# Optimization experiments

Measured on AMD Instinct MI355X. Metric: run time of the kernel, lower is better.

Reference implementation:

```python
import jax, jax.numpy as jnp
import numpy as np

D = 196; NCH = 64; H = 8; DH = 64; INNER = H * DH; MLP = 784; SEQ = 65


def _ln(x, g, b, eps=1e-5):
    m = x.mean(-1, keepdims=True)
    v = x.var(-1, keepdims=True)
    return (x - m) / jnp.sqrt(v + eps) * g + b


def setup_inputs() -> dict:
    key = jax.random.key(0)
    ks = jax.random.split(key, 12)
    f = jax.random.normal
    return dict(
        x=f(ks[0], (1, SEQ, D), dtype=jnp.float32),
        tokens=f(ks[1], (1, D), dtype=jnp.float32),
        x_pe=f(ks[2], (1, NCH, D), dtype=jnp.float32),
        conv_k=f(ks[3], (3, 3), dtype=jnp.float32) * 0.3,   # Conv2d(1,1,3) kernel
        bn_g=jnp.ones(()), bn_b=jnp.zeros(()), bn_rm=jnp.zeros(()), bn_rv=jnp.ones(()),
        fc_w1=f(ks[4], (NCH, 12)) * 0.1,
        fc_w2=f(ks[5], (12, NCH)) * 0.1,
        ln1_g=jnp.ones((D,)), ln1_b=jnp.zeros((D,)),
        ln2_g=jnp.ones((D,)), ln2_b=jnp.zeros((D,)),
        w_qkv=f(ks[6], (D, 3 * INNER)) * 0.05,
        w_out=f(ks[7], (INNER, D)) * 0.05, b_out=jnp.zeros((D,)),
        ff_w1=f(ks[8], (D, MLP)) * 0.05, ff_b1=jnp.zeros((MLP,)),
        ff_w2=f(ks[9], (MLP, D)) * 0.05, ff_b2=jnp.zeros((D,)),
    )


def reference(x, tokens, x_pe, conv_k, bn_g, bn_b, bn_rm, bn_rv,
              fc_w1, fc_w2, ln1_g, ln1_b, ln2_g, ln2_b,
              w_qkv, w_out, b_out, ff_w1, ff_b1, ff_w2, ff_b2):
    # --- per-channel Conv2d(1,1,3,p=1)+BN+ReLU, batched over all 64 rows ---
    # Each row is (1,1,1,196): height 1 with pad 1 means the top/bottom kernel
    # rows only touch zero padding, so only the middle kernel row contributes
    # -> equivalent to a 1D conv with kernel conv_k[1].
    rows = x_pe[0]                      # [64,196]
    km = conv_k[1]                      # [3]
    xp = jnp.pad(rows, ((0, 0), (1, 1)))
    conv = km[0] * xp[:, :D] + km[1] * xp[:, 1:D + 1] + km[2] * xp[:, 2:D + 2]
    bn = (conv - bn_rm) / jnp.sqrt(bn_rv + 1e-5) * bn_g + bn_b
    a = jax.nn.relu(bn)                 # [64,196]  (== x_AfterConv / a)

    # --- sort-based suppress/excitation channel gating ---
    b1 = a.mean(-1)                     # [64] adaptive avg pool
    val = jnp.sort(b1)
    idx = jnp.argsort(b1)
    middle = jnp.where((val.max() < 0) | (val.min() > 0),
                       jnp.int32(32), jnp.argmax(val > 0).astype(jnp.int32))
    rank = jnp.argsort(idx)             # rank of each channel in ascending order
    sup = rank < middle                 # channels in idx[:middle]
    l_s = middle.astype(b1.dtype)
    l_e = (NCH - middle).astype(b1.dtype)
    b2 = jnp.where(sup,
                   b1 - 1.0 / (1.0 + jnp.power(l_s, b1)),
                   b1 + 1.0 / (1.0 + jnp.power(l_e, -b1)))

    c = jax.nn.sigmoid(jax.nn.relu(b2 @ fc_w1) @ fc_w2)   # [64]
    x_att = a * c[:, None]                                  # [64,196]
    x_att = jnp.concatenate([x_att, tokens.reshape(1, D)], axis=0)[None]  # [1,65,196]

    # --- PreNorm attention ---
    h = _ln(x, ln1_g, ln1_b)
    qkv = h @ w_qkv
    q, k, v = jnp.split(qkv, 3, axis=-1)
    def heads(t):
        return t.reshape(1, SEQ, H, DH).transpose(0, 2, 1, 3)  # b h n d
    q, k, v = heads(q), heads(k), heads(v)
    attn = jax.nn.softmax(jnp.einsum('bhnd,bhmd->bhnm', q, k) * (DH ** -0.5), axis=-1)
    o = jnp.einsum('bhnm,bhmd->bhnd', attn, v).transpose(0, 2, 1, 3).reshape(1, SEQ, INNER)
    x = o @ w_out + b_out + x + x_att

    # --- PreNorm feed-forward ---
    h2 = _ln(x, ln2_g, ln2_b)
    x = (jax.nn.gelu(h2 @ ff_w1 + ff_b1, approximate=False) @ ff_w2 + ff_b2) + x
    return x
```

## Files before the change

### kernel.cpp

```cpp
#include <hip/hip_runtime.h>
#include <math.h>

#define D 196
#define NCH 64
#define NH 8
#define DHD 64
#define INNER 512
#define MLP 784
#define SEQ 65

__device__ __forceinline__ float bsum(float v, float* red) {
    for (int off = 32; off > 0; off >>= 1) v += __shfl_down(v, off, 64);
    int lane = threadIdx.x & 63, wid = threadIdx.x >> 6;
    if (lane == 0) red[wid] = v;
    __syncthreads();
    float s = red[0] + red[1] + red[2] + red[3];
    __syncthreads();
    return s;
}

__global__ void __launch_bounds__(256) k1(const float* __restrict__ x_pe,
        const float* __restrict__ conv_k, const float* __restrict__ bn_g,
        const float* __restrict__ bn_b, const float* __restrict__ bn_rm,
        const float* __restrict__ bn_rv, const float* __restrict__ x,
        const float* __restrict__ ln1_g, const float* __restrict__ ln1_b,
        const float* __restrict__ w_qkv,
        float* __restrict__ a, float* __restrict__ b1, float* __restrict__ qkv,
        float* __restrict__ x2, float* __restrict__ out) {
    __shared__ float red[4];
    __shared__ float h[D];
    __shared__ float ps[256];
    int b = blockIdx.x, t = threadIdx.x;
    if (b < NCH) {
        const float* row = x_pe + b * D;
        float val = 0.f;
        if (t < D) {
            float km0 = conv_k[3], km1 = conv_k[4], km2 = conv_k[5];
            float inv = rsqrtf(bn_rv[0] + 1e-5f);
            float l = (t > 0) ? row[t - 1] : 0.f;
            float m = row[t];
            float r = (t < D - 1) ? row[t + 1] : 0.f;
            float conv = km0 * l + km1 * m + km2 * r;
            float bn = (conv - bn_rm[0]) * inv * bn_g[0] + bn_b[0];
            val = fmaxf(bn, 0.f);
            a[b * D + t] = val;
        }
        float tot = bsum(val, red);
        if (t == 0) b1[b] = tot * (1.f / (float)D);
    } else if (b < 844) {
        int qb = b - NCH;
        int n = qb / 12, cg = qb % 12;
        const float* row = x + n * D;
        float v = (t < D) ? row[t] : 0.f;
        float mean = bsum(v, red) * (1.f / (float)D);
        float d = (t < D) ? (v - mean) : 0.f;
        float var = bsum(d * d, red) * (1.f / (float)D);
        float rinv = rsqrtf(var + 1e-5f);
        if (t < D) h[t] = d * rinv * ln1_g[t] + ln1_b[t];
        __syncthreads();
        int half = t >> 7, lt = t & 127;
        int col = cg * 128 + lt;
        const float* wp = w_qkv + (half * 98) * 1536 + col;
        const float* hp = h + half * 98;
        float acc = 0.f;
#pragma unroll 14
        for (int i = 0; i < 98; i++) acc += hp[i] * wp[i * 1536];
        ps[t] = acc;
        __syncthreads();
        if (t < 128) qkv[n * 1536 + cg * 128 + t] = ps[t] + ps[t + 128];
    } else {
        for (int i = t; i < SEQ * D; i += 256) { x2[i] = 0.f; out[i] = 0.f; }
    }
}

__global__ void __launch_bounds__(256) k2(const float* __restrict__ b1,
        const float* __restrict__ fc_w1, const float* __restrict__ fc_w2,
        const float* __restrict__ qkv, float* __restrict__ c, float* __restrict__ o) {
    __shared__ float smem[544];
    int b = blockIdx.x, t = threadIdx.x;
    if (b == 0) {
        float* sb1 = smem;
        float* sb2 = smem + 64;
        float* hid = smem + 128;
        if (t < NCH) sb1[t] = b1[t];
        __syncthreads();
        if (t < NCH) {
            float v = sb1[t];
            float mx = -1e30f, mn = 1e30f;
            int cle = 0, rank = 0;
            for (int j = 0; j < NCH; j++) {
                float w = sb1[j];
                mx = fmaxf(mx, w);
                mn = fminf(mn, w);
                if (w <= 0.f) cle++;
                if (w < v || (w == v && j < t)) rank++;
            }
            int middle;
            if (mx < 0.f || mn > 0.f) middle = 32;
            else if (mx <= 0.f) middle = 0;
            else middle = cle;
            float b2;
            if (rank < middle) {
                float ls = (float)middle;
                b2 = v - 1.f / (1.f + powf(ls, v));
            } else {
                float le = (float)(NCH - middle);
                b2 = v + 1.f / (1.f + powf(le, -v));
            }
            sb2[t] = b2;
        }
        __syncthreads();
        if (t < 12) {
            float s = 0.f;
            for (int j = 0; j < NCH; j++) s += sb2[j] * fc_w1[j * 12 + t];
            hid[t] = fmaxf(s, 0.f);
        }
        __syncthreads();
        if (t < NCH) {
            float s = 0.f;
            for (int k = 0; k < 12; k++) s += hid[k] * fc_w2[k * NCH + t];
            c[t] = 1.f / (1.f + expf(-s));
        }
    } else {
        int w = t >> 6, lane = t & 63;
        int task = (b - 1) * 4 + w;
        int n = task >> 3, hh = task & 7;
        float* q = smem + w * 64;
        float* pp = smem + 256 + w * 66;
        q[lane] = qkv[n * 1536 + hh * DHD + lane];
        __syncthreads();
        const float4* q4 = (const float4*)q;
        const float scale = 0.125f;
        for (int m = lane; m < SEQ; m += 64) {
            const float4* kr = (const float4*)(qkv + m * 1536 + INNER + hh * DHD);
            float s = 0.f;
#pragma unroll
            for (int i = 0; i < 16; i++) {
                float4 kv = kr[i];
                float4 qv = q4[i];
                s += qv.x * kv.x + qv.y * kv.y + qv.z * kv.z + qv.w * kv.w;
            }
            pp[m] = s * scale;
        }
        __syncthreads();
        float mx = -1e30f;
#pragma unroll 5
        for (int m = 0; m < SEQ; m++) mx = fmaxf(mx, pp[m]);
        __syncthreads();
        for (int m = lane; m < SEQ; m += 64) pp[m] = expf(pp[m] - mx);
        __syncthreads();
        float sum = 0.f;
#pragma unroll 5
        for (int m = 0; m < SEQ; m++) sum += pp[m];
        float rs = 1.f / sum;
        float acc = 0.f;
#pragma unroll 8
        for (int m = 0; m < SEQ; m++)
            acc += pp[m] * qkv[m * 1536 + 2 * INNER + hh * DHD + lane];
        o[n * INNER + hh * DHD + lane] = acc * rs;
    }
}

__global__ void __launch_bounds__(256) k3(const float* __restrict__ o,
        const float* __restrict__ w_out, const float* __restrict__ b_out,
        const float* __restrict__ x, const float* __restrict__ a,
        const float* __restrict__ c, const float* __restrict__ tokens,
        float* __restrict__ x2) {
    __shared__ float st[128];
    int n = blockIdx.x, kc = blockIdx.y, t = threadIdx.x;
    if (t < 128) st[t] = o[n * INNER + kc * 128 + t];
    __syncthreads();
    if (t < D) {
        const float* wp = w_out + (kc * 128) * D + t;
        float acc = 0.f;
#pragma unroll 16
        for (int i = 0; i < 128; i++) acc += st[i] * wp[i * D];
        if (kc == 0) {
            float att = (n < NCH) ? a[n * D + t] * c[n] : tokens[t];
            acc += b_out[t] + x[n * D + t] + att;
        }
        atomicAdd(&x2[n * D + t], acc);
    }
}

__global__ void __launch_bounds__(256) k4(const float* __restrict__ x2,
        const float* __restrict__ ln2_g, const float* __restrict__ ln2_b,
        const float* __restrict__ ff_w1, const float* __restrict__ ff_b1,
        float* __restrict__ tb) {
    __shared__ float red[4];
    __shared__ float h[D];
    __shared__ float ps[256];
    int n = blockIdx.x, cg = blockIdx.y, t = threadIdx.x;
    const float* row = x2 + n * D;
    float v = (t < D) ? row[t] : 0.f;
    float mean = bsum(v, red) * (1.f / (float)D);
    float d = (t < D) ? (v - mean) : 0.f;
    float var = bsum(d * d, red) * (1.f / (float)D);
    float rinv = rsqrtf(var + 1e-5f);
    if (t < D) h[t] = d * rinv * ln2_g[t] + ln2_b[t];
    __syncthreads();
    int half = t >> 7, lt = t & 127;
    float acc = 0.f;
    if (lt < 98) {
        int col = cg * 98 + lt;
        const float* wp = ff_w1 + (half * 98) * MLP + col;
        const float* hp = h + half * 98;
        acc = (half == 0) ? ff_b1[col] : 0.f;
#pragma unroll 14
        for (int i = 0; i < 98; i++) acc += hp[i] * wp[i * MLP];
    }
    ps[t] = acc;
    __syncthreads();
    if (t < 98) {
        float s = ps[t] + ps[t + 128];
        float gl = 0.5f * s * (1.f + erff(s * 0.70710678118f));
        tb[n * MLP + cg * 98 + t] = gl;
    }
}

__global__ void __launch_bounds__(256) k5(const float* __restrict__ tb,
        const float* __restrict__ ff_w2, const float* __restrict__ ff_b2,
        const float* __restrict__ x2, float* __restrict__ out) {
    __shared__ float st[98];
    int n = blockIdx.x, kc = blockIdx.y, t = threadIdx.x;
    if (t < 98) st[t] = tb[n * MLP + kc * 98 + t];
    __syncthreads();
    if (t < D) {
        const float* wp = ff_w2 + (kc * 98) * D + t;
        float acc = 0.f;
#pragma unroll 14
        for (int i = 0; i < 98; i++) acc += st[i] * wp[i * D];
        if (kc == 0) acc += ff_b2[t] + x2[n * D + t];
        atomicAdd(&out[n * D + t], acc);
    }
}

extern "C" void kernel_launch(void* const* d_in, const int* in_sizes, int n_in,
                              void* d_out, int out_size, void* d_ws, size_t ws_size,
                              hipStream_t stream) {
    const float* x      = (const float*)d_in[0];
    const float* tokens = (const float*)d_in[1];
    const float* x_pe   = (const float*)d_in[2];
    const float* conv_k = (const float*)d_in[3];
    const float* bn_g   = (const float*)d_in[4];
    const float* bn_b   = (const float*)d_in[5];
    const float* bn_rm  = (const float*)d_in[6];
    const float* bn_rv  = (const float*)d_in[7];
    const float* fc_w1  = (const float*)d_in[8];
    const float* fc_w2  = (const float*)d_in[9];
    const float* ln1_g  = (const float*)d_in[10];
    const float* ln1_b  = (const float*)d_in[11];
    const float* ln2_g  = (const float*)d_in[12];
    const float* ln2_b  = (const float*)d_in[13];
    const float* w_qkv  = (const float*)d_in[14];
    const float* w_out  = (const float*)d_in[15];
    const float* b_out  = (const float*)d_in[16];
    const float* ff_w1  = (const float*)d_in[17];
    const float* ff_b1  = (const float*)d_in[18];
    const float* ff_w2  = (const float*)d_in[19];
    const float* ff_b2  = (const float*)d_in[20];
    float* out = (float*)d_out;

    float* ws = (float*)d_ws;
    float* a    = ws;
    float* b1   = ws + 12544;
    float* cc   = ws + 12608;
    float* qkv  = ws + 12672;
    float* o    = ws + 112512;
    float* x2   = ws + 145792;
    float* tb   = ws + 158532;

    k1<<<845, 256, 0, stream>>>(x_pe, conv_k, bn_g, bn_b, bn_rm, bn_rv,
                                x, ln1_g, ln1_b, w_qkv, a, b1, qkv, x2, out);
    k2<<<131, 256, 0, stream>>>(b1, fc_w1, fc_w2, qkv, cc, o);
    k3<<<dim3(SEQ, 4), 256, 0, stream>>>(o, w_out, b_out, x, a, cc, tokens, x2);
    k4<<<dim3(SEQ, 8), 256, 0, stream>>>(x2, ln2_g, ln2_b, ff_w1, ff_b1, tb);
    k5<<<dim3(SEQ, 8), 256, 0, stream>>>(tb, ff_w2, ff_b2, x2, out);
}
```

Before: 130.7 us.

## Fuse attention with output projection and vectorize GEMV loops with float2

```diff
diff --git a/kernel.cpp b/kernel.cpp
--- a/kernel.cpp
+++ b/kernel.cpp
@@ -26,12 +26,14 @@
         const float* __restrict__ ln1_g, const float* __restrict__ ln1_b,
         const float* __restrict__ w_qkv,
         float* __restrict__ a, float* __restrict__ b1, float* __restrict__ qkv,
-        float* __restrict__ x2, float* __restrict__ out) {
+        float* __restrict__ out) {
     __shared__ float red[4];
     __shared__ float h[D];
-    __shared__ float ps[256];
+    __shared__ float ps[512];
     int b = blockIdx.x, t = threadIdx.x;
     if (b < NCH) {
+        int zi = b * 200 + t;
+        if (t < 200 && zi < SEQ * D) out[zi] = 0.f;
         const float* row = x_pe + b * D;
         float val = 0.f;
         if (t < D) {
@@ -47,7 +49,7 @@
         }
         float tot = bsum(val, red);
         if (t == 0) b1[b] = tot * (1.f / (float)D);
-    } else if (b < 844) {
+    } else {
         int qb = b - NCH;
         int n = qb / 12, cg = qb % 12;
         const float* row = x + n * D;
@@ -58,30 +60,40 @@
         float rinv = rsqrtf(var + 1e-5f);
         if (t < D) h[t] = d * rinv * ln1_g[t] + ln1_b[t];
         __syncthreads();
-        int half = t >> 7, lt = t & 127;
-        int col = cg * 128 + lt;
-        const float* wp = w_qkv + (half * 98) * 1536 + col;
-        const float* hp = h + half * 98;
-        float acc = 0.f;
-#pragma unroll 14
-        for (int i = 0; i < 98; i++) acc += hp[i] * wp[i * 1536];
-        ps[t] = acc;
-        __syncthreads();
-        if (t < 128) qkv[n * 1536 + cg * 128 + t] = ps[t] + ps[t + 128];
-    } else {
-        for (int i = t; i < SEQ * D; i += 256) { x2[i] = 0.f; out[i] = 0.f; }
-    }
-}
-
-__global__ void __launch_bounds__(256) k2(const float* __restrict__ b1,
+        int qq = t >> 6, lt = t & 63;
+        int c0 = cg * 128 + lt * 2;
+        const float* wp = w_qkv + (qq * 49) * 1536 + c0;
+        const float* hp = h + qq * 49;
+        float a0 = 0.f, a1 = 0.f;
+#pragma unroll
+        for (int i = 0; i < 49; i++) {
+            float2 w2 = *(const float2*)(wp + i * 1536);
+            float hv = hp[i];
+            a0 += hv * w2.x;
+            a1 += hv * w2.y;
+        }
+        ps[qq * 128 + lt * 2] = a0;
+        ps[qq * 128 + lt * 2 + 1] = a1;
+        __syncthreads();
+        if (t < 64) {
+            float s0 = ps[t * 2] + ps[128 + t * 2] + ps[256 + t * 2] + ps[384 + t * 2];
+            float s1 = ps[t * 2 + 1] + ps[129 + t * 2] + ps[257 + t * 2] + ps[385 + t * 2];
+            float2 o2 = make_float2(s0, s1);
+            *(float2*)(qkv + n * 1536 + cg * 128 + t * 2) = o2;
+        }
+    }
+}
+
+__global__ void __launch_bounds__(512) k2(const float* __restrict__ b1,
         const float* __restrict__ fc_w1, const float* __restrict__ fc_w2,
-        const float* __restrict__ qkv, float* __restrict__ c, float* __restrict__ o) {
-    __shared__ float smem[544];
+        const float* __restrict__ qkv, const float* __restrict__ w_out,
+        const float* __restrict__ b_out, const float* __restrict__ x,
+        float* __restrict__ c, float* __restrict__ x2) {
     int b = blockIdx.x, t = threadIdx.x;
-    if (b == 0) {
-        float* sb1 = smem;
-        float* sb2 = smem + 64;
-        float* hid = smem + 128;
+    if (b == SEQ) {
+        __shared__ float sb1[NCH];
+        __shared__ float sb2[NCH];
+        __shared__ float hid[12];
         if (t < NCH) sb1[t] = b1[t];
         __syncthreads();
         if (t < NCH) {
@@ -121,117 +133,163 @@
             for (int k = 0; k < 12; k++) s += hid[k] * fc_w2[k * NCH + t];
             c[t] = 1.f / (1.f + expf(-s));
         }
-    } else {
-        int w = t >> 6, lane = t & 63;
-        int task = (b - 1) * 4 + w;
-        int n = task >> 3, hh = task & 7;
-        float* q = smem + w * 64;
-        float* pp = smem + 256 + w * 66;
-        q[lane] = qkv[n * 1536 + hh * DHD + lane];
-        __syncthreads();
-        const float4* q4 = (const float4*)q;
-        const float scale = 0.125f;
-        for (int m = lane; m < SEQ; m += 64) {
-            const float4* kr = (const float4*)(qkv + m * 1536 + INNER + hh * DHD);
-            float s = 0.f;
-#pragma unroll
-            for (int i = 0; i < 16; i++) {
-                float4 kv = kr[i];
-                float4 qv = q4[i];
-                s += qv.x * kv.x + qv.y * kv.y + qv.z * kv.z + qv.w * kv.w;
-            }
-            pp[m] = s * scale;
-        }
-        __syncthreads();
-        float mx = -1e30f;
-#pragma unroll 5
-        for (int m = 0; m < SEQ; m++) mx = fmaxf(mx, pp[m]);
-        __syncthreads();
-        for (int m = lane; m < SEQ; m += 64) pp[m] = expf(pp[m] - mx);
-        __syncthreads();
-        float sum = 0.f;
-#pragma unroll 5
-        for (int m = 0; m < SEQ; m++) sum += pp[m];
-        float rs = 1.f / sum;
-        float acc = 0.f;
-#pragma unroll 8
-        for (int m = 0; m < SEQ; m++)
-            acc += pp[m] * qkv[m * 1536 + 2 * INNER + hh * DHD + lane];
-        o[n * INNER + hh * DHD + lane] = acc * rs;
-    }
-}
-
-__global__ void __launch_bounds__(256) k3(const float* __restrict__ o,
-        const float* __restrict__ w_out, const float* __restrict__ b_out,
-        const float* __restrict__ x, const float* __restrict__ a,
-        const float* __restrict__ c, const float* __restrict__ tokens,
-        float* __restrict__ x2) {
-    __shared__ float st[128];
-    int n = blockIdx.x, kc = blockIdx.y, t = threadIdx.x;
-    if (t < 128) st[t] = o[n * INNER + kc * 128 + t];
-    __syncthreads();
-    if (t < D) {
-        const float* wp = w_out + (kc * 128) * D + t;
-        float acc = 0.f;
+        return;
+    }
+    __shared__ float sq[512];
+    __shared__ float pp[8 * 80];
+    __shared__ float so[512];
+    __shared__ float ps[784];
+    int n = b;
+    int w = t >> 6, L = t & 63;
+    sq[t] = qkv[n * 1536 + t];
+    __syncthreads();
+    const float scale = 0.125f;
+    const float4* kr = (const float4*)(qkv + L * 1536 + INNER + w * DHD);
+    const float4* q4 = (const float4*)(sq + w * DHD);
+    float s = 0.f;
+#pragma unroll
+    for (int i = 0; i < 16; i++) {
+        float4 kv = kr[i];
+        float4 qv = q4[i];
+        s += qv.x * kv.x + qv.y * kv.y + qv.z * kv.z + qv.w * kv.w;
+    }
+    float sL = s * scale;
+    float t64 = sq[w * DHD + L] * qkv[64 * 1536 + INNER + w * DHD + L];
+#pragma unroll
+    for (int off = 1; off < 64; off <<= 1) t64 += __shfl_xor(t64, off, 64);
+    float s64 = t64 * scale;
+    float mx = sL;
+#pragma unroll
+    for (int off = 1; off < 64; off <<= 1) mx = fmaxf(mx, __shfl_xor(mx, off, 64));
+    mx = fmaxf(mx, s64);
+    float e = expf(sL - mx);
+    float e64 = expf(s64 - mx);
+    float esum = e;
+#pragma unroll
+    for (int off = 1; off < 64; off <<= 1) esum += __shfl_xor(esum, off, 64);
+    esum += e64;
+    float rs = 1.f / esum;
+    pp[w * 80 + L] = e;
+    if (L == 0) pp[w * 80 + 64] = e64;
+    __syncthreads();
+    float acc = 0.f;
+#pragma unroll 13
+    for (int m = 0; m < SEQ; m++)
+        acc += pp[w * 80 + m] * qkv[m * 1536 + 2 * INNER + w * DHD + L];
+    so[w * DHD + L] = acc * rs;
+    __syncthreads();
+    if (t < 392) {
+        int qq = t / 98, p = t - qq * 98;
+        const float* wp = w_out + (qq * 128) * D + 2 * p;
+        const float* op = so + qq * 128;
+        float a0 = 0.f, a1 = 0.f;
 #pragma unroll 16
-        for (int i = 0; i < 128; i++) acc += st[i] * wp[i * D];
-        if (kc == 0) {
-            float att = (n < NCH) ? a[n * D + t] * c[n] : tokens[t];
-            acc += b_out[t] + x[n * D + t] + att;
-        }
-        atomicAdd(&x2[n * D + t], acc);
-    }
-}
-
-__global__ void __launch_bounds__(256) k4(const float* __restrict__ x2,
+        for (int i = 0; i < 128; i++) {
+            float2 w2 = *(const float2*)(wp + i * D);
+            float ov = op[i];
+            a0 += ov * w2.x;
+            a1 += ov * w2.y;
+        }
+        ps[qq * 196 + 2 * p] = a0;
+        ps[qq * 196 + 2 * p + 1] = a1;
+    }
+    __syncthreads();
+    if (t < 98) {
+        float s0 = ps[2 * t] + ps[196 + 2 * t] + ps[392 + 2 * t] + ps[588 + 2 * t];
+        float s1 = ps[2 * t + 1] + ps[197 + 2 * t] + ps[393 + 2 * t] + ps[589 + 2 * t];
+        float2 xr = *(const float2*)(x + n * D + 2 * t);
+        float2 br = *(const float2*)(b_out + 2 * t);
+        float2 o2 = make_float2(s0 + xr.x + br.x, s1 + xr.y + br.y);
+        *(float2*)(x2 + n * D + 2 * t) = o2;
+    }
+}
+
+__global__ void __launch_bounds__(256) k3(const float* __restrict__ x2,
+        const float* __restrict__ a, const float* __restrict__ c,
+        const float* __restrict__ tokens,
         const float* __restrict__ ln2_g, const float* __restrict__ ln2_b,
         const float* __restrict__ ff_w1, const float* __restrict__ ff_b1,
         float* __restrict__ tb) {
     __shared__ float red[4];
     __shared__ float h[D];
-    __shared__ float ps[256];
+    __shared__ float ps[392];
     int n = blockIdx.x, cg = blockIdx.y, t = threadIdx.x;
-    const float* row = x2 + n * D;
-    float v = (t < D) ? row[t] : 0.f;
+    float v = 0.f;
+    if (t < D) {
+        float att = (n < NCH) ? a[n * D + t] * c[n] : tokens[t];
+        v = x2[n * D + t] + att;
+    }
     float mean = bsum(v, red) * (1.f / (float)D);
     float d = (t < D) ? (v - mean) : 0.f;
     float var = bsum(d * d, red) * (1.f / (float)D);
     float rinv = rsqrtf(var + 1e-5f);
     if (t < D) h[t] = d * rinv * ln2_g[t] + ln2_b[t];
     __syncthreads();
-    int half = t >> 7, lt = t & 127;
-    float acc = 0.f;
-    if (lt < 98) {
-        int col = cg * 98 + lt;
-        const float* wp = ff_w1 + (half * 98) * MLP + col;
-        const float* hp = h + half * 98;
-        acc = (half == 0) ? ff_b1[col] : 0.f;
-#pragma unroll 14
-        for (int i = 0; i < 98; i++) acc += hp[i] * wp[i * MLP];
-    }
-    ps[t] = acc;
-    __syncthreads();
-    if (t < 98) {
-        float s = ps[t] + ps[t + 128];
-        float gl = 0.5f * s * (1.f + erff(s * 0.70710678118f));
-        tb[n * MLP + cg * 98 + t] = gl;
-    }
-}
-
-__global__ void __launch_bounds__(256) k5(const float* __restrict__ tb,
+    if (t < D) {
+        int qq = t / 49, p = t - qq * 49;
+        int c0 = cg * 98 + 2 * p;
+        const float* wp = ff_w1 + (qq * 49) * MLP + c0;
+        const float* hp = h + qq * 49;
+        float a0 = 0.f, a1 = 0.f;
+#pragma unroll
+        for (int i = 0; i < 49; i++) {
+            float2 w2 = *(const float2*)(wp + i * MLP);
+            float hv = hp[i];
+            a0 += hv * w2.x;
+            a1 += hv * w2.y;
+        }
+        if (qq == 0) { a0 += ff_b1[c0]; a1 += ff_b1[c0 + 1]; }
+        ps[qq * 98 + 2 * p] = a0;
+        ps[qq * 98 + 2 * p + 1] = a1;
+    }
+    __syncthreads();
+    if (t < 49) {
+        float s0 = ps[2 * t] + ps[98 + 2 * t] + ps[196 + 2 * t] + ps[294 + 2 * t];
+        float s1 = ps[2 * t + 1] + ps[99 + 2 * t] + ps[197 + 2 * t] + ps[295 + 2 * t];
+        float g0 = 0.5f * s0 * (1.f + erff(s0 * 0.70710678118f));
+        float g1 = 0.5f * s1 * (1.f + erff(s1 * 0.70710678118f));
+        *(float2*)(tb + n * MLP + cg * 98 + 2 * t) = make_float2(g0, g1);
+    }
+}
+
+__global__ void __launch_bounds__(256) k4(const float* __restrict__ tb,
         const float* __restrict__ ff_w2, const float* __restrict__ ff_b2,
-        const float* __restrict__ x2, float* __restrict__ out) {
+        const float* __restrict__ x2, const float* __restrict__ a,
+        const float* __restrict__ c, const float* __restrict__ tokens,
+        float* __restrict__ out) {
     __shared__ float st[98];
+    __shared__ float ps[392];
     int n = blockIdx.x, kc = blockIdx.y, t = threadIdx.x;
     if (t < 98) st[t] = tb[n * MLP + kc * 98 + t];
     __syncthreads();
     if (t < D) {
-        const float* wp = ff_w2 + (kc * 98) * D + t;
-        float acc = 0.f;
-#pragma unroll 14
-        for (int i = 0; i < 98; i++) acc += st[i] * wp[i * D];
-        if (kc == 0) acc += ff_b2[t] + x2[n * D + t];
-        atomicAdd(&out[n * D + t], acc);
+        int hh = t / 98, p = t - hh * 98;
+        const float* wp = ff_w2 + (kc * 98 + hh * 49) * D + 2 * p;
+        const float* sp = st + hh * 49;
+        float a0 = 0.f, a1 = 0.f;
+#pragma unroll
+        for (int i = 0; i < 49; i++) {
+            float2 w2 = *(const float2*)(wp + i * D);
+            float sv = sp[i];
+            a0 += sv * w2.x;
+            a1 += sv * w2.y;
+        }
+        ps[hh * 196 + 2 * p] = a0;
+        ps[hh * 196 + 2 * p + 1] = a1;
+    }
+    __syncthreads();
+    if (t < 98) {
+        float s0 = ps[2 * t] + ps[196 + 2 * t];
+        float s1 = ps[2 * t + 1] + ps[197 + 2 * t];
+        if (kc == 0) {
+            int c0 = 2 * t;
+            float att0 = (n < NCH) ? a[n * D + c0] * c[n] : tokens[c0];
+            float att1 = (n < NCH) ? a[n * D + c0 + 1] * c[n] : tokens[c0 + 1];
+            s0 += ff_b2[c0] + x2[n * D + c0] + att0;
+            s1 += ff_b2[c0 + 1] + x2[n * D + c0 + 1] + att1;
+        }
+        atomicAdd(&out[n * D + 2 * t], s0);
+        atomicAdd(&out[n * D + 2 * t + 1], s1);
     }
 }
 
@@ -266,14 +324,13 @@
     float* b1   = ws + 12544;
     float* cc   = ws + 12608;
     float* qkv  = ws + 12672;
-    float* o    = ws + 112512;
-    float* x2   = ws + 145792;
-    float* tb   = ws + 158532;
-
-    k1<<<845, 256, 0, stream>>>(x_pe, conv_k, bn_g, bn_b, bn_rm, bn_rv,
-                                x, ln1_g, ln1_b, w_qkv, a, b1, qkv, x2, out);
-    k2<<<131, 256, 0, stream>>>(b1, fc_w1, fc_w2, qkv, cc, o);
-    k3<<<dim3(SEQ, 4), 256, 0, stream>>>(o, w_out, b_out, x, a, cc, tokens, x2);
-    k4<<<dim3(SEQ, 8), 256, 0, stream>>>(x2, ln2_g, ln2_b, ff_w1, ff_b1, tb);
-    k5<<<dim3(SEQ, 8), 256, 0, stream>>>(tb, ff_w2, ff_b2, x2, out);
-}
+    float* x2   = ws + 112512;
+    float* tb   = ws + 125252;
+
+    k1<<<844, 256, 0, stream>>>(x_pe, conv_k, bn_g, bn_b, bn_rm, bn_rv,
+                                x, ln1_g, ln1_b, w_qkv, a, b1, qkv, out);
+    k2<<<SEQ + 1, 512, 0, stream>>>(b1, fc_w1, fc_w2, qkv, w_out, b_out, x, cc, x2);
+    k3<<<dim3(SEQ, 8), 256, 0, stream>>>(x2, a, cc, tokens, ln2_g, ln2_b,
+                                         ff_w1, ff_b1, tb);
+    k4<<<dim3(SEQ, 8), 256, 0, stream>>>(tb, ff_w2, ff_b2, x2, a, cc, tokens, out);
+}
```

New measurement: 130.1 us. Within noise of the previous version (-0.4%).
